# Optimization experiments

Hardware: AMD Instinct MI355X
Metric: run time of the kernel (lower is better)

Reference implementation:

```python
import math
import jax, jax.numpy as jnp
import numpy as np
from jax import lax


def _l2n(v, eps=1e-12):
    return v / (jnp.linalg.norm(v) + eps)


def _sn(w_bar, u, v):
    # one power iteration (as in SpectralNorm with power_iterations=1)
    h = w_bar.shape[0]
    wm = w_bar.reshape(h, -1)
    v = _l2n(wm.T @ u)
    u = _l2n(wm @ v)
    u = lax.stop_gradient(u)  # u, v are updated via .data in torch (no grad)
    v = lax.stop_gradient(v)
    sigma = u @ (wm @ v)
    return w_bar / sigma


def _conv(x, w, stride, pad):
    return lax.conv_general_dilated(
        x, w, (stride, stride), [(pad, pad), (pad, pad)],
        dimension_numbers=('NCHW', 'OIHW', 'NCHW'))


def _make_blur_kernel():
    k = jnp.array([1., 3., 3., 1.], jnp.float32)
    k2 = k[None, :] * k[:, None]
    return k2 / k2.sum()  # 4x4, sums to 1


def _blur(x, k2, pad):
    # upfirdn2d with up=1, down=1: pad then depthwise FIR filter
    C = x.shape[1]
    xp = jnp.pad(x, ((0, 0), (0, 0), (pad[0], pad[1]), (pad[0], pad[1])))
    w = jnp.tile(k2[None, None], (C, 1, 1, 1))  # [C,1,4,4]
    return lax.conv_general_dilated(
        xp, w, (1, 1), 'VALID', feature_group_count=C,
        dimension_numbers=('NCHW', 'OIHW', 'NCHW'))


def setup_inputs() -> dict:
    key = jax.random.key(0)
    ks = jax.random.split(key, 12)
    Cin, Cout = 256, 512
    x = jax.random.normal(ks[0], (16, Cin, 64, 64), jnp.float32)
    w1_bar = jax.random.normal(ks[1], (Cin, Cin, 3, 3), jnp.float32) * 0.05
    u1 = _l2n(jax.random.normal(ks[2], (Cin,), jnp.float32))
    v1 = _l2n(jax.random.normal(ks[3], (Cin * 9,), jnp.float32))
    b1 = jnp.zeros((Cin,), jnp.float32)
    w2_bar = jax.random.normal(ks[4], (Cout, Cin, 3, 3), jnp.float32) * 0.05
    u2 = _l2n(jax.random.normal(ks[5], (Cout,), jnp.float32))
    v2 = _l2n(jax.random.normal(ks[6], (Cin * 9,), jnp.float32))
    b2 = jnp.zeros((Cout,), jnp.float32)
    ws_bar = jax.random.normal(ks[7], (Cout, Cin, 1, 1), jnp.float32) * 0.05
    us = _l2n(jax.random.normal(ks[8], (Cout,), jnp.float32))
    vs = _l2n(jax.random.normal(ks[9], (Cin,), jnp.float32))
    return dict(x=x, w1_bar=w1_bar, u1=u1, v1=v1, b1=b1,
                w2_bar=w2_bar, u2=u2, v2=v2, b2=b2,
                ws_bar=ws_bar, us=us, vs=vs)


def reference(x, w1_bar, u1, v1, b1, w2_bar, u2, v2, b2, ws_bar, us, vs):
    k2 = _make_blur_kernel()
    # conv1: 3x3 same-res, SN conv + bias + LeakyReLU(0.2)
    out = _conv(x, _sn(w1_bar, u1, v1), 1, 1) + b1[None, :, None, None]
    out = jax.nn.leaky_relu(out, 0.2)
    # conv2: blur pad=(2,2) then 3x3 stride-2 SN conv + bias + LeakyReLU
    out = _blur(out, k2, (2, 2))
    out = _conv(out, _sn(w2_bar, u2, v2), 2, 0) + b2[None, :, None, None]
    out = jax.nn.leaky_relu(out, 0.2)
    # skip: blur pad=(1,1) then 1x1 stride-2 SN conv (no bias, no act)
    skip = _blur(x, k2, (1, 1))
    skip = _conv(skip, _sn(ws_bar, us, vs), 2, 0)
    return (out + skip) / math.sqrt(2)
```

## Files before the change

kernel.cpp:

```cpp
#include <hip/hip_runtime.h>
#include <math.h>

typedef unsigned short u16;
typedef __attribute__((ext_vector_type(8))) unsigned short ushort8;
typedef __attribute__((ext_vector_type(4))) unsigned short u16x4;
typedef __attribute__((ext_vector_type(8))) short short8;
typedef __attribute__((ext_vector_type(4))) float f32x4;

__device__ __forceinline__ float b2f(u16 v) {
    unsigned u = ((unsigned)v) << 16; float f; __builtin_memcpy(&f, &u, 4); return f;
}
__device__ __forceinline__ u16 f2b(float f) {
    unsigned u; __builtin_memcpy(&u, &f, 4);
    u = (u + 0x7fffu + ((u >> 16) & 1u)) >> 16;
    return (u16)u;
}
__device__ __forceinline__ float ldin(const void* p, int i, int flag) {
    return flag ? ((const float*)p)[i] : b2f(((const u16*)p)[i]);
}
__device__ __forceinline__ void split2(float x, u16& h, u16& l) {
    h = f2b(x);
    l = f2b(x - b2f(h));
}
__device__ __forceinline__ ushort8 zero8() {
    ushort8 z;
#pragma unroll
    for (int i = 0; i < 8; ++i) z[i] = 0;
    return z;
}
__device__ __forceinline__ void tile_barrier() {
    asm volatile("s_waitcnt lgkmcnt(0)" ::: "memory");
    __builtin_amdgcn_s_barrier();
    asm volatile("" ::: "memory");
}

__global__ void detect_kernel(const unsigned* __restrict__ xw, int* __restrict__ flag) {
    __shared__ int red[4];
    int tid = threadIdx.x, lane = tid & 63, wid = tid >> 6;
    int cnt = 0;
    for (int i = 0; i < 16; ++i) {
        unsigned w = xw[tid * 16 + i];
        unsigned e = (w >> 23) & 0xFF;
        if (e >= 77u && e <= 157u) ++cnt;
    }
    for (int o = 32; o; o >>= 1) cnt += __shfl_down(cnt, o, 64);
    if (lane == 0) red[wid] = cnt;
    __syncthreads();
    if (tid == 0) flag[0] = (red[0] + red[1] + red[2] + red[3] >= 2048) ? 1 : 0;
}

__global__ void sig_init_kernel(float* __restrict__ t, float* __restrict__ ns) {
    int i = blockIdx.x * 256 + threadIdx.x;
    if (i < 4864) t[i] = 0.f;
    if (i < 3) ns[i] = 0.f;
}

__global__ void sig_t_kernel(const void* __restrict__ w1, const void* __restrict__ u1,
                             const void* __restrict__ w2, const void* __restrict__ u2,
                             const void* __restrict__ wsb, const void* __restrict__ us,
                             const int* __restrict__ flagp, float* __restrict__ t) {
    __shared__ float ush[64];
    int blk = blockIdx.x;
    int flag = flagp[0];
    const void* W; const void* U; int m, toff, jc, ic;
    if (blk < 36)       { W = w1;  U = u1; m = 2304; toff = 0;    jc = blk % 9; ic = blk / 9; }
    else if (blk < 108) { int r = blk - 36;  W = w2;  U = u2; m = 2304; toff = 2304; jc = r % 9; ic = r / 9; }
    else                { int r = blk - 108; W = wsb; U = us; m = 256;  toff = 4608; jc = 0;     ic = r; }
    int tid = threadIdx.x;
    if (tid < 64) ush[tid] = ldin(U, ic * 64 + tid, flag);
    __syncthreads();
    int j = jc * 256 + tid;
    float acc = 0.f;
    int base = ic * 64 * m + j;
    for (int ii = 0; ii < 64; ++ii) acc += ldin(W, base + ii * m, flag) * ush[ii];
    atomicAdd(&t[toff + j], acc);
}

__global__ void sig_norm_kernel(float* __restrict__ t, float* __restrict__ ntinv) {
    __shared__ float red[4];
    int b = blockIdx.x;
    int m = (b == 2) ? 256 : 2304;
    int toff = b * 2304;
    int tid = threadIdx.x, lane = tid & 63, wid = tid >> 6;
    float s = 0.f;
    for (int j = tid; j < m; j += 256) { float v = t[toff + j]; s += v * v; }
    for (int o = 32; o; o >>= 1) s += __shfl_down(s, o, 64);
    if (lane == 0) red[wid] = s;
    __syncthreads();
    if (tid == 0) ntinv[b] = 1.f / (sqrtf(red[0] + red[1] + red[2] + red[3]) + 1e-12f);
}

__global__ void sig_s_kernel(const void* __restrict__ w1, const void* __restrict__ w2,
                             const void* __restrict__ wsb, const int* __restrict__ flagp,
                             const float* __restrict__ t, const float* __restrict__ ntinv,
                             float* __restrict__ ns) {
    int flag = flagp[0];
    int wg = blockIdx.x * 4 + (threadIdx.x >> 6);
    int lane = threadIdx.x & 63;
    const void* W; int m, toff, i, b;
    if (wg < 256)      { W = w1;  m = 2304; toff = 0;    i = wg;       b = 0; }
    else if (wg < 768) { W = w2;  m = 2304; toff = 2304; i = wg - 256; b = 1; }
    else               { W = wsb; m = 256;  toff = 4608; i = wg - 768; b = 2; }
    float acc = 0.f;
    int base = i * m;
    for (int j = lane; j < m; j += 64) acc += ldin(W, base + j, flag) * t[toff + j];
    for (int o = 32; o; o >>= 1) acc += __shfl_down(acc, o, 64);
    if (lane == 0) { float s = acc * ntinv[b]; atomicAdd(&ns[b], s * s); }
}

__global__ void sig_fin_kernel(const float* __restrict__ ns, float* __restrict__ inv_sigma) {
    int b = threadIdx.x;
    if (b < 3) { float s2 = ns[b]; float s = sqrtf(s2); inv_sigma[b] = (s + 1e-12f) / s2; }
}

__global__ void wprep_kernel(const void* __restrict__ w1b, const void* __restrict__ w2b,
                             const void* __restrict__ wsb,
                             const void* __restrict__ b1,  const void* __restrict__ b2,
                             const float* __restrict__ inv_sigma, const int* __restrict__ flagp,
                             u16* __restrict__ w1h, u16* __restrict__ w1l,
                             u16* __restrict__ w2h, u16* __restrict__ w2l,
                             u16* __restrict__ wsh, u16* __restrict__ wsl,
                             float* __restrict__ b1f, float* __restrict__ b2f_) {
    int idx = blockIdx.x * 256 + threadIdx.x;
    int flag = flagp[0];
    float s0 = inv_sigma[0], s1 = inv_sigma[1], s2 = inv_sigma[2];
    if (idx < 589824) {
        int kyx = idx / 65536; int rem = idx - kyx * 65536;
        int co = rem >> 8, ci = rem & 255;
        float w = ldin(w1b, ((co << 8) + ci) * 9 + kyx, flag) * s0;
        split2(w, w1h[idx], w1l[idx]);
    } else if (idx < 589824 + 1179648) {
        int i2 = idx - 589824;
        int kyx = i2 / 131072; int rem = i2 - kyx * 131072;
        int co = rem >> 8, ci = rem & 255;
        float w = ldin(w2b, ((co << 8) + ci) * 9 + kyx, flag) * s1;
        split2(w, w2h[i2], w2l[i2]);
    } else if (idx < 1900544) {
        int i3 = idx - 1769472;
        float w = ldin(wsb, i3, flag) * s2;
        split2(w, wsh[i3], wsl[i3]);
    } else if (idx < 1900544 + 256) {
        b1f[idx - 1900544] = ldin(b1, idx - 1900544, flag);
    } else if (idx < 1900544 + 768) {
        b2f_[idx - 1900800] = ldin(b2, idx - 1900800, flag);
    }
}

__global__ void transpose_kernel(const void* __restrict__ x, u16* __restrict__ xh,
                                 u16* __restrict__ xl,
                                 const int* __restrict__ flagp, int n0) {
    __shared__ float tile[32][65];
    int flag = flagp[0];
    int ny  = blockIdx.x;
    int ci0 = blockIdx.y * 32;
    int nl = ny >> 6, y = ny & 63;
    int t = threadIdx.x;
    int ci_l = t >> 3, x8 = (t & 7) * 8;
    int base = ((n0 + nl) * 256 + ci0 + ci_l) * 4096 + y * 64 + x8;
    if (flag) {
        const float* xf = (const float*)x;
        float4 v0 = *(const float4*)&xf[base];
        float4 v1 = *(const float4*)&xf[base + 4];
        tile[ci_l][x8 + 0] = v0.x; tile[ci_l][x8 + 1] = v0.y;
        tile[ci_l][x8 + 2] = v0.z; tile[ci_l][x8 + 3] = v0.w;
        tile[ci_l][x8 + 4] = v1.x; tile[ci_l][x8 + 5] = v1.y;
        tile[ci_l][x8 + 6] = v1.z; tile[ci_l][x8 + 7] = v1.w;
    } else {
        const u16* xb = (const u16*)x;
        ushort8 v = *(const ushort8*)&xb[base];
#pragma unroll
        for (int k = 0; k < 8; ++k) tile[ci_l][x8 + k] = b2f(v[k]);
    }
    __syncthreads();
    int x_l = t >> 2, oc = (t & 3) * 8;
    size_t o = ((size_t)ny * 64 + x_l) * 256 + ci0 + oc;
    ushort8 h, l;
#pragma unroll
    for (int k = 0; k < 8; ++k) {
        u16 hh, ll; split2(tile[oc + k][x_l], hh, ll);
        h[k] = hh; l[k] = ll;
    }
    *(ushort8*)&xh[o] = h;
    *(ushort8*)&xl[o] = l;
}

__device__ __constant__ float BW[4] = {0.125f, 0.375f, 0.375f, 0.125f};

__global__ void blur1_kernel(const u16* __restrict__ a1h, const u16* __restrict__ a1l,
                             u16* __restrict__ bh, u16* __restrict__ bl) {
    int idx = blockIdx.x * 256 + threadIdx.x;
    int ch = (idx & 31) * 8;
    int rem = idx >> 5;
    int xq = rem % 65; rem /= 65;
    int yq = rem % 65;
    int n  = rem / 65;
    float acc[8];
#pragma unroll
    for (int k = 0; k < 8; ++k) acc[k] = 0.f;
#pragma unroll
    for (int i = 0; i < 4; ++i) {
        int yy = yq + i - 2;
        if ((unsigned)yy >= 64u) continue;
#pragma unroll
        for (int j = 0; j < 4; ++j) {
            int xx = xq + j - 2;
            if ((unsigned)xx >= 64u) continue;
            float w = BW[i] * BW[j];
            size_t g = ((size_t)((n * 64 + yy) * 64 + xx) << 8) + ch;
            ushort8 vh = *(const ushort8*)&a1h[g];
            ushort8 vl = *(const ushort8*)&a1l[g];
#pragma unroll
            for (int k = 0; k < 8; ++k) acc[k] += w * (b2f(vh[k]) + b2f(vl[k]));
        }
    }
    ushort8 h, l;
#pragma unroll
    for (int k = 0; k < 8; ++k) {
        u16 hh, ll; split2(acc[k], hh, ll);
        h[k] = hh; l[k] = ll;
    }
    size_t o = ((size_t)((n * 65 + yq) * 65 + xq) << 8) + ch;
    *(ushort8*)&bh[o] = h;
    *(ushort8*)&bl[o] = l;
}

__global__ void blursample_kernel(const u16* __restrict__ xh, const u16* __restrict__ xl,
                                  u16* __restrict__ sh, u16* __restrict__ sl) {
    int idx = blockIdx.x * 256 + threadIdx.x;
    int ch = (idx & 31) * 8;
    int rem = idx >> 5;
    int xo = rem & 31;
    int yo = (rem >> 5) & 31;
    int n  = rem >> 10;
    float acc[8];
#pragma unroll
    for (int k = 0; k < 8; ++k) acc[k] = 0.f;
#pragma unroll
    for (int i = 0; i < 4; ++i) {
        int yy = 2 * yo + i - 1;
        if ((unsigned)yy >= 64u) continue;
#pragma unroll
        for (int j = 0; j < 4; ++j) {
            int xx = 2 * xo + j - 1;
            if ((unsigned)xx >= 64u) continue;
            float w = BW[i] * BW[j];
            size_t g = ((size_t)((n * 64 + yy) * 64 + xx) << 8) + ch;
            ushort8 vh = *(const ushort8*)&xh[g];
            ushort8 vl = *(const ushort8*)&xl[g];
#pragma unroll
            for (int k = 0; k < 8; ++k) acc[k] += w * (b2f(vh[k]) + b2f(vl[k]));
        }
    }
    ushort8 h, l;
#pragma unroll
    for (int k = 0; k < 8; ++k) {
        u16 hh, ll; split2(acc[k], hh, ll);
        h[k] = hh; l[k] = ll;
    }
    size_t o = ((size_t)((n * 32 + yo) * 32 + xo) << 8) + ch;
    *(ushort8*)&sh[o] = h;
    *(ushort8*)&sl[o] = l;
}

#define LDK 40

#define C1_LOAD(IT, RAH0, RAH1, RAL0, RAL1, RBH0, RBH1, RBL0, RBL1) {          \
    int p_ = (IT) >> 3, kc_ = (IT) & 7;                                        \
    const u16* wh_ = w1h + (size_t)p_ * 65536;                                 \
    const u16* wl_ = w1l + (size_t)p_ * 65536;                                 \
    size_t gs_ = (size_t)(co_base + ra) * 256 + kc_ * 32 + ka;                 \
    RAH0 = *(const ushort8*)&wh_[gs_];                                         \
    RAH1 = *(const ushort8*)&wh_[gs_ + 8];                                     \
    if (DOLO) { RAL0 = *(const ushort8*)&wl_[gs_];                             \
                RAL1 = *(const ushort8*)&wl_[gs_ + 8]; }                       \
    int dy_ = p_ / 3 - 1, dx_ = p_ % 3 - 1;                                    \
    int yy_ = y0 + (ra >> 6) + dy_, xx_ = (ra & 63) + dx_;                     \
    if ((unsigned)yy_ < 64u && (unsigned)xx_ < 64u) {                          \
        size_t g_ = ((size_t)((n * 64 + yy_) * 64 + xx_) << 8) + kc_ * 32 + ka;\
        RBH0 = *(const ushort8*)&xh[g_];                                       \
        RBH1 = *(const ushort8*)&xh[g_ + 8];                                   \
        if (DOLO) { RBL0 = *(const ushort8*)&xl[g_];                           \
                    RBL1 = *(const ushort8*)&xl[g_ + 8]; }                     \
    } else {                                                                   \
        RBH0 = zero8(); RBH1 = zero8();                                        \
        if (DOLO) { RBL0 = zero8(); RBL1 = zero8(); }                          \
    }                                                                          \
}

template <bool DOLO>
__device__ __forceinline__ void conv1_body(
        const u16* __restrict__ xh, const u16* __restrict__ xl,
        const u16* __restrict__ w1h, const u16* __restrict__ w1l,
        const float* __restrict__ b1f, u16* __restrict__ a1h, u16* __restrict__ a1l,
        u16* Ah, u16* Al, u16* Bh, u16* Bl) {
    int tid = threadIdx.x, lane = tid & 63, wid = tid >> 6;
    int col = lane & 15, quad = lane >> 4;
    int wco = (wid >> 1) * 64, wsp = (wid & 1) * 64;
    int bidx = blockIdx.x;
    int sp_blk = (bidx & 7) * 32 + (bidx >> 3);
    int sp_base = sp_blk * 128;
    int co_base = blockIdx.y * 128;
    int n  = sp_base >> 12;
    int y0 = (sp_base & 4095) >> 6;
    int ra = tid >> 1, ka = (tid & 1) * 16;

    f32x4 acc[4][4];
#pragma unroll
    for (int i = 0; i < 4; ++i)
#pragma unroll
        for (int j = 0; j < 4; ++j) acc[i][j] = (f32x4){0.f, 0.f, 0.f, 0.f};

    ushort8 nAh0, nAh1, nAl0, nAl1, nBh0, nBh1, nBl0, nBl1;
    C1_LOAD(0, nAh0, nAh1, nAl0, nAl1, nBh0, nBh1, nBl0, nBl1);

    for (int it = 0; it < 72; ++it) {
        __syncthreads();
        *(ushort8*)&Ah[ra * LDK + ka]     = nAh0;
        *(ushort8*)&Ah[ra * LDK + ka + 8] = nAh1;
        if (DOLO) {
            *(ushort8*)&Al[ra * LDK + ka]     = nAl0;
            *(ushort8*)&Al[ra * LDK + ka + 8] = nAl1;
        }
        *(ushort8*)&Bh[ra * LDK + ka]     = nBh0;
        *(ushort8*)&Bh[ra * LDK + ka + 8] = nBh1;
        if (DOLO) {
            *(ushort8*)&Bl[ra * LDK + ka]     = nBl0;
            *(ushort8*)&Bl[ra * LDK + ka + 8] = nBl1;
        }
        int itn = (it + 1 < 72) ? it + 1 : it;
        C1_LOAD(itn, nAh0, nAh1, nAl0, nAl1, nBh0, nBh1, nBl0, nBl1);
        tile_barrier();
        short8 ah[4], al[4];
#pragma unroll
        for (int tm = 0; tm < 4; ++tm) {
            ah[tm] = *(const short8*)&Ah[(wco + tm * 16 + col) * LDK + quad * 8];
            if (DOLO) al[tm] = *(const short8*)&Al[(wco + tm * 16 + col) * LDK + quad * 8];
        }
#pragma unroll
        for (int tn = 0; tn < 4; ++tn) {
            short8 bh = *(const short8*)&Bh[(wsp + tn * 16 + col) * LDK + quad * 8];
            short8 bl;
            if (DOLO) bl = *(const short8*)&Bl[(wsp + tn * 16 + col) * LDK + quad * 8];
#pragma unroll
            for (int tm = 0; tm < 4; ++tm) {
                acc[tm][tn] = __builtin_amdgcn_mfma_f32_16x16x32_bf16(ah[tm], bh, acc[tm][tn], 0, 0, 0);
                if (DOLO) {
                    acc[tm][tn] = __builtin_amdgcn_mfma_f32_16x16x32_bf16(ah[tm], bl, acc[tm][tn], 0, 0, 0);
                    acc[tm][tn] = __builtin_amdgcn_mfma_f32_16x16x32_bf16(al[tm], bh, acc[tm][tn], 0, 0, 0);
                }
            }
        }
    }
#pragma unroll
    for (int tm = 0; tm < 4; ++tm) {
        int cog = co_base + wco + tm * 16 + quad * 4;
        float4 bias = *(const float4*)&b1f[cog];
        float bb[4] = {bias.x, bias.y, bias.z, bias.w};
#pragma unroll
        for (int tn = 0; tn < 4; ++tn) {
            int sp = sp_base + wsp + tn * 16 + col;
            u16x4 oh, ol;
#pragma unroll
            for (int r = 0; r < 4; ++r) {
                float v = acc[tm][tn][r] + bb[r];
                v = v > 0.f ? v : 0.2f * v;
                u16 hh, ll; split2(v, hh, ll);
                oh[r] = hh; ol[r] = ll;
            }
            *(u16x4*)&a1h[((size_t)sp << 8) + cog] = oh;
            *(u16x4*)&a1l[((size_t)sp << 8) + cog] = ol;
        }
    }
}

__global__ __launch_bounds__(256, 2) void conv1_kernel(
        const u16* __restrict__ xh, const u16* __restrict__ xl,
        const u16* __restrict__ w1h, const u16* __restrict__ w1l,
        const float* __restrict__ b1f, u16* __restrict__ a1h, u16* __restrict__ a1l,
        const int* __restrict__ flagp) {
    __shared__ u16 Ah[128 * LDK];
    __shared__ u16 Al[128 * LDK];
    __shared__ u16 Bh[128 * LDK];
    __shared__ u16 Bl[128 * LDK];
    if (flagp[0]) conv1_body<true >(xh, xl, w1h, w1l, b1f, a1h, a1l, Ah, Al, Bh, Bl);
    else          conv1_body<false>(xh, xl, w1h, w1l, b1f, a1h, a1l, Ah, Al, Bh, Bl);
}

#define C2_LOAD(IT, RAH, RAL, RBH0, RBH1, RBL0, RBL1) {                        \
    int p_ = (IT) >> 3, kc_ = (IT) & 7; int ci0_ = kc_ * 32;                   \
    const u16* wh_ = (p_ < 9) ? w2h + (size_t)p_ * 131072 : wsh;               \
    const u16* wl_ = (p_ < 9) ? w2l + (size_t)p_ * 131072 : wsl;               \
    size_t gs_ = (size_t)(co_base + ra) * 256 + ci0_ + ka;                     \
    RAH = *(const ushort8*)&wh_[gs_];                                          \
    if (DOLO) RAL = *(const ushort8*)&wl_[gs_];                                \
    const u16 *sh_, *sl_; size_t g_;                                           \
    if (p_ < 9) {                                                              \
        int ky_ = p_ / 3, kx_ = p_ % 3;                                        \
        int yi_ = 2 * (yo0 + (r_st >> 5)) + ky_;                               \
        int xi_ = 2 * (r_st & 31) + kx_;                                       \
        g_ = (size_t)((n * 65 + yi_) * 65 + xi_) * 256 + ci0_ + k_st;          \
        sh_ = bl1h; sl_ = bl1l;                                                \
    } else {                                                                   \
        g_ = ((size_t)(sp_base + r_st) << 8) + ci0_ + k_st;                    \
        sh_ = skh; sl_ = skl;                                                  \
    }                                                                          \
    RBH0 = *(const ushort8*)&sh_[g_];                                          \
    RBH1 = *(const ushort8*)&sh_[g_ + 8];                                      \
    if (DOLO) { RBL0 = *(const ushort8*)&sl_[g_];                              \
                RBL1 = *(const ushort8*)&sl_[g_ + 8]; }                        \
}

template <bool DOLO>
__device__ __forceinline__ void conv2_body(
        const u16* __restrict__ bl1h, const u16* __restrict__ bl1l,
        const u16* __restrict__ skh,  const u16* __restrict__ skl,
        const u16* __restrict__ w2h, const u16* __restrict__ w2l,
        const u16* __restrict__ wsh, const u16* __restrict__ wsl,
        const float* __restrict__ b2f_, void* __restrict__ out, int n0,
        u16* Ah, u16* Al, u16* Bh, u16* Bl, int flag) {
    int tid = threadIdx.x, lane = tid & 63, wid = tid >> 6;
    int col = lane & 15, quad = lane >> 4;
    int wco = (wid >> 1) * 32, wsp = (wid & 1) * 64;
    int b = blockIdx.x;
    int img    = b & 7;
    int r      = b >> 3;
    int co_blk = r & 7;
    int sp_in  = r >> 3;
    int sp_base = img * 1024 + sp_in * 128;
    int co_base = co_blk * 64;
    int n   = img;
    int yo0 = sp_in * 4;
    int r_st = tid >> 1, k_st = (tid & 1) * 16;
    int ra = tid >> 2, ka = (tid & 3) * 8;

    f32x4 acc[2][4], accs[2][4];
#pragma unroll
    for (int i = 0; i < 2; ++i)
#pragma unroll
        for (int j = 0; j < 4; ++j) {
            acc[i][j]  = (f32x4){0.f, 0.f, 0.f, 0.f};
            accs[i][j] = (f32x4){0.f, 0.f, 0.f, 0.f};
        }

    ushort8 nAh, nAl, nBh0, nBh1, nBl0, nBl1;
    C2_LOAD(0, nAh, nAl, nBh0, nBh1, nBl0, nBl1);

    for (int it = 0; it < 80; ++it) {
        int p = it >> 3;
        __syncthreads();
        *(ushort8*)&Ah[ra * LDK + ka] = nAh;
        if (DOLO) *(ushort8*)&Al[ra * LDK + ka] = nAl;
        *(ushort8*)&Bh[r_st * LDK + k_st]     = nBh0;
        *(ushort8*)&Bh[r_st * LDK + k_st + 8] = nBh1;
        if (DOLO) {
            *(ushort8*)&Bl[r_st * LDK + k_st]     = nBl0;
            *(ushort8*)&Bl[r_st * LDK + k_st + 8] = nBl1;
        }
        int itn = (it + 1 < 80) ? it + 1 : it;
        C2_LOAD(itn, nAh, nAl, nBh0, nBh1, nBl0, nBl1);
        tile_barrier();
        short8 ah[2], al[2];
#pragma unroll
        for (int tm = 0; tm < 2; ++tm) {
            ah[tm] = *(const short8*)&Ah[(wco + tm * 16 + col) * LDK + quad * 8];
            if (DOLO) al[tm] = *(const short8*)&Al[(wco + tm * 16 + col) * LDK + quad * 8];
        }
        if (p < 9) {
#pragma unroll
            for (int tn = 0; tn < 4; ++tn) {
                short8 bh = *(const short8*)&Bh[(wsp + tn * 16 + col) * LDK + quad * 8];
                short8 bl;
                if (DOLO) bl = *(const short8*)&Bl[(wsp + tn * 16 + col) * LDK + quad * 8];
#pragma unroll
                for (int tm = 0; tm < 2; ++tm) {
                    acc[tm][tn] = __builtin_amdgcn_mfma_f32_16x16x32_bf16(ah[tm], bh, acc[tm][tn], 0, 0, 0);
                    if (DOLO) {
                        acc[tm][tn] = __builtin_amdgcn_mfma_f32_16x16x32_bf16(ah[tm], bl, acc[tm][tn], 0, 0, 0);
                        acc[tm][tn] = __builtin_amdgcn_mfma_f32_16x16x32_bf16(al[tm], bh, acc[tm][tn], 0, 0, 0);
                    }
                }
            }
        } else {
#pragma unroll
            for (int tn = 0; tn < 4; ++tn) {
                short8 bh = *(const short8*)&Bh[(wsp + tn * 16 + col) * LDK + quad * 8];
                short8 bl;
                if (DOLO) bl = *(const short8*)&Bl[(wsp + tn * 16 + col) * LDK + quad * 8];
#pragma unroll
                for (int tm = 0; tm < 2; ++tm) {
                    accs[tm][tn] = __builtin_amdgcn_mfma_f32_16x16x32_bf16(ah[tm], bh, accs[tm][tn], 0, 0, 0);
                    if (DOLO) {
                        accs[tm][tn] = __builtin_amdgcn_mfma_f32_16x16x32_bf16(ah[tm], bl, accs[tm][tn], 0, 0, 0);
                        accs[tm][tn] = __builtin_amdgcn_mfma_f32_16x16x32_bf16(al[tm], bh, accs[tm][tn], 0, 0, 0);
                    }
                }
            }
        }
    }
    const float RS2 = 0.70710678118654752f;
#pragma unroll
    for (int tm = 0; tm < 2; ++tm) {
        int cog = co_base + wco + tm * 16 + quad * 4;
        float4 bias = *(const float4*)&b2f_[cog];
        float bb[4] = {bias.x, bias.y, bias.z, bias.w};
#pragma unroll
        for (int tn = 0; tn < 4; ++tn) {
            int sp  = sp_base + wsp + tn * 16 + col;
            int ng  = n0 + (sp >> 10);
            int rem = sp & 1023;
            size_t ob = ((size_t)ng * 512 + cog) * 1024 + rem;
#pragma unroll
            for (int r2 = 0; r2 < 4; ++r2) {
                float v = acc[tm][tn][r2] + bb[r2];
                v = v > 0.f ? v : 0.2f * v;
                v = (v + accs[tm][tn][r2]) * RS2;
                if (flag) ((float*)out)[ob + (size_t)r2 * 1024] = v;
                else      ((u16*)out)[ob + (size_t)r2 * 1024]   = f2b(v);
            }
        }
    }
}

__global__ __launch_bounds__(256, 2) void conv2_kernel(
        const u16* __restrict__ bl1h, const u16* __restrict__ bl1l,
        const u16* __restrict__ skh,  const u16* __restrict__ skl,
        const u16* __restrict__ w2h, const u16* __restrict__ w2l,
        const u16* __restrict__ wsh, const u16* __restrict__ wsl,
        const float* __restrict__ b2f_, const int* __restrict__ flagp,
        void* __restrict__ out, int n0) {
    __shared__ u16 Ah[64 * LDK];
    __shared__ u16 Al[64 * LDK];
    __shared__ u16 Bh[128 * LDK];
    __shared__ u16 Bl[128 * LDK];
    int flag = flagp[0];
    if (flag) conv2_body<true >(bl1h, bl1l, skh, skl, w2h, w2l, wsh, wsl, b2f_, out, n0, Ah, Al, Bh, Bl, flag);
    else      conv2_body<false>(bl1h, bl1l, skh, skl, w2h, w2l, wsh, wsl, b2f_, out, n0, Ah, Al, Bh, Bl, flag);
}

extern "C" void kernel_launch(void* const* d_in, const int* in_sizes, int n_in,
                              void* d_out, int out_size, void* d_ws, size_t ws_size,
                              hipStream_t stream) {
    const void* x   = d_in[0];
    const void* w1b = d_in[1];
    const void* u1  = d_in[2];
    const void* b1  = d_in[4];
    const void* w2b = d_in[5];
    const void* u2  = d_in[6];
    const void* b2  = d_in[8];
    const void* wsb = d_in[9];
    const void* us  = d_in[10];

    char* ws = (char*)d_ws;
    int*   flag      = (int*)(ws);
    float* inv_sigma = (float*)(ws + 64);
    float* b1f       = (float*)(ws + 1024);
    float* b2fp      = (float*)(ws + 2048);
    u16* w1h = (u16*)(ws + 4096);
    u16* w1l = (u16*)(ws + 1183744);
    u16* w2h = (u16*)(ws + 2363392);
    u16* w2l = (u16*)(ws + 4722688);
    u16* wsh = (u16*)(ws + 7081984);
    u16* wsl = (u16*)(ws + 7344128);
    u16* xth  = (u16*)(ws + 7606272);
    u16* xtl  = (u16*)(ws + 7606272 + 16777216);
    u16* bl1h = (u16*)(ws + 7606272);
    u16* bl1l = (u16*)(ws + 7606272 + 17305600);
    u16* a1h = (u16*)(ws + 42217472);
    u16* a1l = (u16*)(ws + 42217472 + 16777216);
    u16* skh = (u16*)(ws + 75771904);
    u16* skl = (u16*)(ws + 75771904 + 4194304);
    float* tvec  = (float*)(ws + 7606272);
    float* ntinv = (float*)(ws + 7606272 + 19456);
    float* ns    = (float*)(ws + 7606272 + 19520);

    detect_kernel<<<1, 256, 0, stream>>>((const unsigned*)x, flag);
    sig_init_kernel<<<19, 256, 0, stream>>>(tvec, ns);
    sig_t_kernel<<<116, 256, 0, stream>>>(w1b, u1, w2b, u2, wsb, us, flag, tvec);
    sig_norm_kernel<<<3, 256, 0, stream>>>(tvec, ntinv);
    sig_s_kernel<<<320, 256, 0, stream>>>(w1b, w2b, wsb, flag, tvec, ntinv, ns);
    sig_fin_kernel<<<1, 64, 0, stream>>>(ns, inv_sigma);
    wprep_kernel<<<7427, 256, 0, stream>>>(w1b, w2b, wsb, b1, b2, inv_sigma, flag,
                                           w1h, w1l, w2h, w2l, wsh, wsl, b1f, b2fp);
    for (int c = 0; c < 2; ++c) {
        int n0 = c * 8;
        transpose_kernel<<<dim3(512, 8), 256, 0, stream>>>(x, xth, xtl, flag, n0);
        blursample_kernel<<<1024, 256, 0, stream>>>(xth, xtl, skh, skl);
        conv1_kernel<<<dim3(256, 2), 256, 0, stream>>>(xth, xtl, w1h, w1l, b1f, a1h, a1l, flag);
        blur1_kernel<<<4225, 256, 0, stream>>>(a1h, a1l, bl1h, bl1l);
        conv2_kernel<<<512, 256, 0, stream>>>(bl1h, bl1l, skh, skl, w2h, w2l,
                                              wsh, wsl, b2fp, flag, d_out, n0);
    }
}
```

Baseline: 653.0 us.

## Double-buffer LDS tiles in conv1 and conv2 with one barrier per step

Splits the shared-memory A/B tiles of both conv kernels into two halves and ping-pongs between them. Fragments for the current step are read, the next tile is written to the other half, and the tile after that is prefetched from global memory, leaving one barrier per iteration instead of two. The MFMA section is wrapped in raised wave priority (s_setprio). This doubles LDS use per block (conv1 goes to about 80KB), which may limit the two-blocks-per-CU occupancy the launch bounds ask for.

```diff
diff --git a/kernel.cpp b/kernel.cpp
--- a/kernel.cpp
+++ b/kernel.cpp
@@ -263,6 +263,7 @@
 }
 
 #define LDK 40
+#define C1_HALF (128 * LDK)
 
 #define C1_LOAD(IT, RAH0, RAH1, RAL0, RAL1, RBH0, RBH1, RBL0, RBL1) {          \
     int p_ = (IT) >> 3, kc_ = (IT) & 7;                                        \
@@ -287,6 +288,21 @@
     }                                                                          \
 }
 
+#define C1_WRITE(OFF) {                                                        \
+    *(ushort8*)&Ah[(OFF) + ra * LDK + ka]     = nAh0;                          \
+    *(ushort8*)&Ah[(OFF) + ra * LDK + ka + 8] = nAh1;                          \
+    if (DOLO) {                                                                \
+        *(ushort8*)&Al[(OFF) + ra * LDK + ka]     = nAl0;                      \
+        *(ushort8*)&Al[(OFF) + ra * LDK + ka + 8] = nAl1;                      \
+    }                                                                          \
+    *(ushort8*)&Bh[(OFF) + ra * LDK + ka]     = nBh0;                          \
+    *(ushort8*)&Bh[(OFF) + ra * LDK + ka + 8] = nBh1;                          \
+    if (DOLO) {                                                                \
+        *(ushort8*)&Bl[(OFF) + ra * LDK + ka]     = nBl0;                      \
+        *(ushort8*)&Bl[(OFF) + ra * LDK + ka + 8] = nBl1;                      \
+    }                                                                          \
+}
+
 template <bool DOLO>
 __device__ __forceinline__ void conv1_body(
         const u16* __restrict__ xh, const u16* __restrict__ xl,
@@ -312,44 +328,40 @@
 
     ushort8 nAh0, nAh1, nAl0, nAl1, nBh0, nBh1, nBl0, nBl1;
     C1_LOAD(0, nAh0, nAh1, nAl0, nAl1, nBh0, nBh1, nBl0, nBl1);
+    C1_WRITE(0);
+    C1_LOAD(1, nAh0, nAh1, nAl0, nAl1, nBh0, nBh1, nBl0, nBl1);
+    tile_barrier();
 
     for (int it = 0; it < 72; ++it) {
-        __syncthreads();
-        *(ushort8*)&Ah[ra * LDK + ka]     = nAh0;
-        *(ushort8*)&Ah[ra * LDK + ka + 8] = nAh1;
-        if (DOLO) {
-            *(ushort8*)&Al[ra * LDK + ka]     = nAl0;
-            *(ushort8*)&Al[ra * LDK + ka + 8] = nAl1;
-        }
-        *(ushort8*)&Bh[ra * LDK + ka]     = nBh0;
-        *(ushort8*)&Bh[ra * LDK + ka + 8] = nBh1;
-        if (DOLO) {
-            *(ushort8*)&Bl[ra * LDK + ka]     = nBl0;
-            *(ushort8*)&Bl[ra * LDK + ka + 8] = nBl1;
-        }
-        int itn = (it + 1 < 72) ? it + 1 : it;
+        const int cur = (it & 1) ? C1_HALF : 0;
+        const int nxt = (it & 1) ? 0 : C1_HALF;
+        short8 ah[4], al[4], bhf[4], blf[4];
+#pragma unroll
+        for (int tm = 0; tm < 4; ++tm) {
+            ah[tm] = *(const short8*)&Ah[cur + (wco + tm * 16 + col) * LDK + quad * 8];
+            if (DOLO) al[tm] = *(const short8*)&Al[cur + (wco + tm * 16 + col) * LDK + quad * 8];
+        }
+#pragma unroll
+        for (int tn = 0; tn < 4; ++tn) {
+            bhf[tn] = *(const short8*)&Bh[cur + (wsp + tn * 16 + col) * LDK + quad * 8];
+            if (DOLO) blf[tn] = *(const short8*)&Bl[cur + (wsp + tn * 16 + col) * LDK + quad * 8];
+        }
+        C1_WRITE(nxt);
+        int itn = (it + 2 < 72) ? it + 2 : 71;
         C1_LOAD(itn, nAh0, nAh1, nAl0, nAl1, nBh0, nBh1, nBl0, nBl1);
-        tile_barrier();
-        short8 ah[4], al[4];
-#pragma unroll
-        for (int tm = 0; tm < 4; ++tm) {
-            ah[tm] = *(const short8*)&Ah[(wco + tm * 16 + col) * LDK + quad * 8];
-            if (DOLO) al[tm] = *(const short8*)&Al[(wco + tm * 16 + col) * LDK + quad * 8];
-        }
-#pragma unroll
-        for (int tn = 0; tn < 4; ++tn) {
-            short8 bh = *(const short8*)&Bh[(wsp + tn * 16 + col) * LDK + quad * 8];
-            short8 bl;
-            if (DOLO) bl = *(const short8*)&Bl[(wsp + tn * 16 + col) * LDK + quad * 8];
+        __builtin_amdgcn_s_setprio(1);
+#pragma unroll
+        for (int tn = 0; tn < 4; ++tn)
 #pragma unroll
             for (int tm = 0; tm < 4; ++tm) {
-                acc[tm][tn] = __builtin_amdgcn_mfma_f32_16x16x32_bf16(ah[tm], bh, acc[tm][tn], 0, 0, 0);
+                acc[tm][tn] = __builtin_amdgcn_mfma_f32_16x16x32_bf16(ah[tm], bhf[tn], acc[tm][tn], 0, 0, 0);
                 if (DOLO) {
-                    acc[tm][tn] = __builtin_amdgcn_mfma_f32_16x16x32_bf16(ah[tm], bl, acc[tm][tn], 0, 0, 0);
-                    acc[tm][tn] = __builtin_amdgcn_mfma_f32_16x16x32_bf16(al[tm], bh, acc[tm][tn], 0, 0, 0);
+                    acc[tm][tn] = __builtin_amdgcn_mfma_f32_16x16x32_bf16(ah[tm], blf[tn], acc[tm][tn], 0, 0, 0);
+                    acc[tm][tn] = __builtin_amdgcn_mfma_f32_16x16x32_bf16(al[tm], bhf[tn], acc[tm][tn], 0, 0, 0);
                 }
             }
-        }
+        __builtin_amdgcn_s_setprio(0);
+        tile_barrier();
     }
 #pragma unroll
     for (int tm = 0; tm < 4; ++tm) {
@@ -378,13 +390,16 @@
         const u16* __restrict__ w1h, const u16* __restrict__ w1l,
         const float* __restrict__ b1f, u16* __restrict__ a1h, u16* __restrict__ a1l,
         const int* __restrict__ flagp) {
-    __shared__ u16 Ah[128 * LDK];
-    __shared__ u16 Al[128 * LDK];
-    __shared__ u16 Bh[128 * LDK];
-    __shared__ u16 Bl[128 * LDK];
+    __shared__ u16 Ah[2 * 128 * LDK];
+    __shared__ u16 Al[2 * 128 * LDK];
+    __shared__ u16 Bh[2 * 128 * LDK];
+    __shared__ u16 Bl[2 * 128 * LDK];
     if (flagp[0]) conv1_body<true >(xh, xl, w1h, w1l, b1f, a1h, a1l, Ah, Al, Bh, Bl);
     else          conv1_body<false>(xh, xl, w1h, w1l, b1f, a1h, a1l, Ah, Al, Bh, Bl);
 }
+
+#define C2_AHALF (64 * LDK)
+#define C2_BHALF (128 * LDK)
 
 #define C2_LOAD(IT, RAH, RAL, RBH0, RBH1, RBL0, RBL1) {                        \
     int p_ = (IT) >> 3, kc_ = (IT) & 7; int ci0_ = kc_ * 32;                   \
@@ -410,6 +425,17 @@
                 RBL1 = *(const ushort8*)&sl_[g_ + 8]; }                        \
 }
 
+#define C2_WRITE(AOFF, BOFF) {                                                 \
+    *(ushort8*)&Ah[(AOFF) + ra * LDK + ka] = nAh;                              \
+    if (DOLO) *(ushort8*)&Al[(AOFF) + ra * LDK + ka] = nAl;                    \
+    *(ushort8*)&Bh[(BOFF) + r_st * LDK + k_st]     = nBh0;                     \
+    *(ushort8*)&Bh[(BOFF) + r_st * LDK + k_st + 8] = nBh1;                     \
+    if (DOLO) {                                                                \
+        *(ushort8*)&Bl[(BOFF) + r_st * LDK + k_st]     = nBl0;                 \
+        *(ushort8*)&Bl[(BOFF) + r_st * LDK + k_st + 8] = nBl1;                 \
+    }                                                                          \
+}
+
 template <bool DOLO>
 __device__ __forceinline__ void conv2_body(
         const u16* __restrict__ bl1h, const u16* __restrict__ bl1l,
@@ -444,58 +470,56 @@
 
     ushort8 nAh, nAl, nBh0, nBh1, nBl0, nBl1;
     C2_LOAD(0, nAh, nAl, nBh0, nBh1, nBl0, nBl1);
+    C2_WRITE(0, 0);
+    C2_LOAD(1, nAh, nAl, nBh0, nBh1, nBl0, nBl1);
+    tile_barrier();
 
     for (int it = 0; it < 80; ++it) {
         int p = it >> 3;
-        __syncthreads();
-        *(ushort8*)&Ah[ra * LDK + ka] = nAh;
-        if (DOLO) *(ushort8*)&Al[ra * LDK + ka] = nAl;
-        *(ushort8*)&Bh[r_st * LDK + k_st]     = nBh0;
-        *(ushort8*)&Bh[r_st * LDK + k_st + 8] = nBh1;
-        if (DOLO) {
-            *(ushort8*)&Bl[r_st * LDK + k_st]     = nBl0;
-            *(ushort8*)&Bl[r_st * LDK + k_st + 8] = nBl1;
-        }
-        int itn = (it + 1 < 80) ? it + 1 : it;
+        const int curA = (it & 1) ? C2_AHALF : 0;
+        const int nxtA = (it & 1) ? 0 : C2_AHALF;
+        const int curB = (it & 1) ? C2_BHALF : 0;
+        const int nxtB = (it & 1) ? 0 : C2_BHALF;
+        short8 ah[2], al[2], bhf[4], blf[4];
+#pragma unroll
+        for (int tm = 0; tm < 2; ++tm) {
+            ah[tm] = *(const short8*)&Ah[curA + (wco + tm * 16 + col) * LDK + quad * 8];
+            if (DOLO) al[tm] = *(const short8*)&Al[curA + (wco + tm * 16 + col) * LDK + quad * 8];
+        }
+#pragma unroll
+        for (int tn = 0; tn < 4; ++tn) {
+            bhf[tn] = *(const short8*)&Bh[curB + (wsp + tn * 16 + col) * LDK + quad * 8];
+            if (DOLO) blf[tn] = *(const short8*)&Bl[curB + (wsp + tn * 16 + col) * LDK + quad * 8];
+        }
+        C2_WRITE(nxtA, nxtB);
+        int itn = (it + 2 < 80) ? it + 2 : 79;
         C2_LOAD(itn, nAh, nAl, nBh0, nBh1, nBl0, nBl1);
-        tile_barrier();
-        short8 ah[2], al[2];
-#pragma unroll
-        for (int tm = 0; tm < 2; ++tm) {
-            ah[tm] = *(const short8*)&Ah[(wco + tm * 16 + col) * LDK + quad * 8];
-            if (DOLO) al[tm] = *(const short8*)&Al[(wco + tm * 16 + col) * LDK + quad * 8];
-        }
+        __builtin_amdgcn_s_setprio(1);
         if (p < 9) {
 #pragma unroll
-            for (int tn = 0; tn < 4; ++tn) {
-                short8 bh = *(const short8*)&Bh[(wsp + tn * 16 + col) * LDK + quad * 8];
-                short8 bl;
-                if (DOLO) bl = *(const short8*)&Bl[(wsp + tn * 16 + col) * LDK + quad * 8];
+            for (int tn = 0; tn < 4; ++tn)
 #pragma unroll
                 for (int tm = 0; tm < 2; ++tm) {
-                    acc[tm][tn] = __builtin_amdgcn_mfma_f32_16x16x32_bf16(ah[tm], bh, acc[tm][tn], 0, 0, 0);
+                    acc[tm][tn] = __builtin_amdgcn_mfma_f32_16x16x32_bf16(ah[tm], bhf[tn], acc[tm][tn], 0, 0, 0);
                     if (DOLO) {
-                        acc[tm][tn] = __builtin_amdgcn_mfma_f32_16x16x32_bf16(ah[tm], bl, acc[tm][tn], 0, 0, 0);
-                        acc[tm][tn] = __builtin_amdgcn_mfma_f32_16x16x32_bf16(al[tm], bh, acc[tm][tn], 0, 0, 0);
+                        acc[tm][tn] = __builtin_amdgcn_mfma_f32_16x16x32_bf16(ah[tm], blf[tn], acc[tm][tn], 0, 0, 0);
+                        acc[tm][tn] = __builtin_amdgcn_mfma_f32_16x16x32_bf16(al[tm], bhf[tn], acc[tm][tn], 0, 0, 0);
                     }
                 }
-            }
         } else {
 #pragma unroll
-            for (int tn = 0; tn < 4; ++tn) {
-                short8 bh = *(const short8*)&Bh[(wsp + tn * 16 + col) * LDK + quad * 8];
-                short8 bl;
-                if (DOLO) bl = *(const short8*)&Bl[(wsp + tn * 16 + col) * LDK + quad * 8];
+            for (int tn = 0; tn < 4; ++tn)
 #pragma unroll
                 for (int tm = 0; tm < 2; ++tm) {
-                    accs[tm][tn] = __builtin_amdgcn_mfma_f32_16x16x32_bf16(ah[tm], bh, accs[tm][tn], 0, 0, 0);
+                    accs[tm][tn] = __builtin_amdgcn_mfma_f32_16x16x32_bf16(ah[tm], bhf[tn], accs[tm][tn], 0, 0, 0);
                     if (DOLO) {
-                        accs[tm][tn] = __builtin_amdgcn_mfma_f32_16x16x32_bf16(ah[tm], bl, accs[tm][tn], 0, 0, 0);
-                        accs[tm][tn] = __builtin_amdgcn_mfma_f32_16x16x32_bf16(al[tm], bh, accs[tm][tn], 0, 0, 0);
+                        accs[tm][tn] = __builtin_amdgcn_mfma_f32_16x16x32_bf16(ah[tm], blf[tn], accs[tm][tn], 0, 0, 0);
+                        accs[tm][tn] = __builtin_amdgcn_mfma_f32_16x16x32_bf16(al[tm], bhf[tn], accs[tm][tn], 0, 0, 0);
                     }
                 }
-            }
-        }
+        }
+        __builtin_amdgcn_s_setprio(0);
+        tile_barrier();
     }
     const float RS2 = 0.70710678118654752f;
 #pragma unroll
@@ -528,10 +552,10 @@
         const u16* __restrict__ wsh, const u16* __restrict__ wsl,
         const float* __restrict__ b2f_, const int* __restrict__ flagp,
         void* __restrict__ out, int n0) {
-    __shared__ u16 Ah[64 * LDK];
-    __shared__ u16 Al[64 * LDK];
-    __shared__ u16 Bh[128 * LDK];
-    __shared__ u16 Bl[128 * LDK];
+    __shared__ u16 Ah[2 * 64 * LDK];
+    __shared__ u16 Al[2 * 64 * LDK];
+    __shared__ u16 Bh[2 * 128 * LDK];
+    __shared__ u16 Bl[2 * 128 * LDK];
     int flag = flagp[0];
     if (flag) conv2_body<true >(bl1h, bl1l, skh, skl, w2h, w2l, wsh, wsl, b2f_, out, n0, Ah, Al, Bh, Bl, flag);
     else      conv2_body<false>(bl1h, bl1l, skh, skl, w2h, w2l, wsh, wsl, b2f_, out, n0, Ah, Al, Bh, Bl, flag);
```

New measurement: 668.9 us. 2.4% more time.

## Double-buffer conv1 LDS tiles with one barrier per K-step and MFMA priority

Applied to the files above, without the earlier changes.

Conv1's LDS tiles are now double-buffered. Each iteration reads its fragments from the current buffer, writes the prefetched registers into the other buffer, issues the global loads two steps ahead, then runs the MFMAs under raised wave priority. This replaces the two barriers per step with one and is meant to overlap global loads and LDS stores with matrix math. The cost is twice the LDS (80 KB per block), which may limit occupancy to the two blocks declared in launch bounds or fewer.

```diff
diff --git a/kernel.cpp b/kernel.cpp
--- a/kernel.cpp
+++ b/kernel.cpp
@@ -263,6 +263,7 @@
 }
 
 #define LDK 40
+#define C1_HALF (128 * LDK)
 
 #define C1_LOAD(IT, RAH0, RAH1, RAL0, RAL1, RBH0, RBH1, RBL0, RBL1) {          \
     int p_ = (IT) >> 3, kc_ = (IT) & 7;                                        \
@@ -287,6 +288,21 @@
     }                                                                          \
 }
 
+#define C1_WRITE(OFF) {                                                        \
+    *(ushort8*)&Ah[(OFF) + ra * LDK + ka]     = nAh0;                          \
+    *(ushort8*)&Ah[(OFF) + ra * LDK + ka + 8] = nAh1;                          \
+    if (DOLO) {                                                                \
+        *(ushort8*)&Al[(OFF) + ra * LDK + ka]     = nAl0;                      \
+        *(ushort8*)&Al[(OFF) + ra * LDK + ka + 8] = nAl1;                      \
+    }                                                                          \
+    *(ushort8*)&Bh[(OFF) + ra * LDK + ka]     = nBh0;                          \
+    *(ushort8*)&Bh[(OFF) + ra * LDK + ka + 8] = nBh1;                          \
+    if (DOLO) {                                                                \
+        *(ushort8*)&Bl[(OFF) + ra * LDK + ka]     = nBl0;                      \
+        *(ushort8*)&Bl[(OFF) + ra * LDK + ka + 8] = nBl1;                      \
+    }                                                                          \
+}
+
 template <bool DOLO>
 __device__ __forceinline__ void conv1_body(
         const u16* __restrict__ xh, const u16* __restrict__ xl,
@@ -312,44 +328,40 @@
 
     ushort8 nAh0, nAh1, nAl0, nAl1, nBh0, nBh1, nBl0, nBl1;
     C1_LOAD(0, nAh0, nAh1, nAl0, nAl1, nBh0, nBh1, nBl0, nBl1);
+    C1_WRITE(0);
+    C1_LOAD(1, nAh0, nAh1, nAl0, nAl1, nBh0, nBh1, nBl0, nBl1);
+    tile_barrier();
 
     for (int it = 0; it < 72; ++it) {
-        __syncthreads();
-        *(ushort8*)&Ah[ra * LDK + ka]     = nAh0;
-        *(ushort8*)&Ah[ra * LDK + ka + 8] = nAh1;
-        if (DOLO) {
-            *(ushort8*)&Al[ra * LDK + ka]     = nAl0;
-            *(ushort8*)&Al[ra * LDK + ka + 8] = nAl1;
-        }
-        *(ushort8*)&Bh[ra * LDK + ka]     = nBh0;
-        *(ushort8*)&Bh[ra * LDK + ka + 8] = nBh1;
-        if (DOLO) {
-            *(ushort8*)&Bl[ra * LDK + ka]     = nBl0;
-            *(ushort8*)&Bl[ra * LDK + ka + 8] = nBl1;
-        }
-        int itn = (it + 1 < 72) ? it + 1 : it;
+        const int cur = (it & 1) ? C1_HALF : 0;
+        const int nxt = (it & 1) ? 0 : C1_HALF;
+        short8 ah[4], al[4], bhf[4], blf[4];
+#pragma unroll
+        for (int tm = 0; tm < 4; ++tm) {
+            ah[tm] = *(const short8*)&Ah[cur + (wco + tm * 16 + col) * LDK + quad * 8];
+            if (DOLO) al[tm] = *(const short8*)&Al[cur + (wco + tm * 16 + col) * LDK + quad * 8];
+        }
+#pragma unroll
+        for (int tn = 0; tn < 4; ++tn) {
+            bhf[tn] = *(const short8*)&Bh[cur + (wsp + tn * 16 + col) * LDK + quad * 8];
+            if (DOLO) blf[tn] = *(const short8*)&Bl[cur + (wsp + tn * 16 + col) * LDK + quad * 8];
+        }
+        C1_WRITE(nxt);
+        int itn = (it + 2 < 72) ? it + 2 : 71;
         C1_LOAD(itn, nAh0, nAh1, nAl0, nAl1, nBh0, nBh1, nBl0, nBl1);
-        tile_barrier();
-        short8 ah[4], al[4];
-#pragma unroll
-        for (int tm = 0; tm < 4; ++tm) {
-            ah[tm] = *(const short8*)&Ah[(wco + tm * 16 + col) * LDK + quad * 8];
-            if (DOLO) al[tm] = *(const short8*)&Al[(wco + tm * 16 + col) * LDK + quad * 8];
-        }
-#pragma unroll
-        for (int tn = 0; tn < 4; ++tn) {
-            short8 bh = *(const short8*)&Bh[(wsp + tn * 16 + col) * LDK + quad * 8];
-            short8 bl;
-            if (DOLO) bl = *(const short8*)&Bl[(wsp + tn * 16 + col) * LDK + quad * 8];
+        __builtin_amdgcn_s_setprio(1);
+#pragma unroll
+        for (int tn = 0; tn < 4; ++tn)
 #pragma unroll
             for (int tm = 0; tm < 4; ++tm) {
-                acc[tm][tn] = __builtin_amdgcn_mfma_f32_16x16x32_bf16(ah[tm], bh, acc[tm][tn], 0, 0, 0);
+                acc[tm][tn] = __builtin_amdgcn_mfma_f32_16x16x32_bf16(ah[tm], bhf[tn], acc[tm][tn], 0, 0, 0);
                 if (DOLO) {
-                    acc[tm][tn] = __builtin_amdgcn_mfma_f32_16x16x32_bf16(ah[tm], bl, acc[tm][tn], 0, 0, 0);
-                    acc[tm][tn] = __builtin_amdgcn_mfma_f32_16x16x32_bf16(al[tm], bh, acc[tm][tn], 0, 0, 0);
+                    acc[tm][tn] = __builtin_amdgcn_mfma_f32_16x16x32_bf16(ah[tm], blf[tn], acc[tm][tn], 0, 0, 0);
+                    acc[tm][tn] = __builtin_amdgcn_mfma_f32_16x16x32_bf16(al[tm], bhf[tn], acc[tm][tn], 0, 0, 0);
                 }
             }
-        }
+        __builtin_amdgcn_s_setprio(0);
+        tile_barrier();
     }
 #pragma unroll
     for (int tm = 0; tm < 4; ++tm) {
@@ -378,10 +390,10 @@
         const u16* __restrict__ w1h, const u16* __restrict__ w1l,
         const float* __restrict__ b1f, u16* __restrict__ a1h, u16* __restrict__ a1l,
         const int* __restrict__ flagp) {
-    __shared__ u16 Ah[128 * LDK];
-    __shared__ u16 Al[128 * LDK];
-    __shared__ u16 Bh[128 * LDK];
-    __shared__ u16 Bl[128 * LDK];
+    __shared__ u16 Ah[2 * 128 * LDK];
+    __shared__ u16 Al[2 * 128 * LDK];
+    __shared__ u16 Bh[2 * 128 * LDK];
+    __shared__ u16 Bl[2 * 128 * LDK];
     if (flagp[0]) conv1_body<true >(xh, xl, w1h, w1l, b1f, a1h, a1l, Ah, Al, Bh, Bl);
     else          conv1_body<false>(xh, xl, w1h, w1l, b1f, a1h, a1l, Ah, Al, Bh, Bl);
 }
```

Measured after the change: 662.4 us. About the same (+1.4%).
